# Kernel tuning notes

Hardware: AMD Instinct MI355X
Metric: run time of the kernel (lower is better)

Reference implementation:

```python
import jax, jax.numpy as jnp
import numpy as np

DIM = 2048
K_DIM = 2048
Q_HEADS = 16
KV_HEADS = 4
HEAD_DIM = DIM // Q_HEADS  # 128
KV_DIM = HEAD_DIM * KV_HEADS
ROPE_THETA = 10000.0


def _rope_cos_sin(seq_len, head_dim):
    inv = 1.0 / (ROPE_THETA ** (np.arange(0, head_dim, 2).astype(np.float32) / head_dim))
    t = np.arange(seq_len, dtype=np.float32)
    freqs = np.outer(t, inv)  # (n, head_dim/2)
    return jnp.asarray(np.cos(freqs)), jnp.asarray(np.sin(freqs))


def _apply_rope(x, cos, sin):
    # x: (b, n, h, d); interleaved complex pairs as in torch.view_as_complex
    b, n, h, d = x.shape
    xr, xi = x[..., 0::2], x[..., 1::2]
    c = cos[None, :, None, :]
    s = sin[None, :, None, :]
    yr = xr * c - xi * s
    yi = xr * s + xi * c
    return jnp.stack([yr, yi], axis=-1).reshape(b, n, h, d)


def setup_inputs() -> dict:
    key = jax.random.key(0)
    ks = jax.random.split(key, 11)
    B, N = 2, 2048
    std_q = DIM ** -0.5
    std_k = K_DIM ** -0.5
    return {
        "query": jax.random.normal(ks[0], (B, N, DIM), jnp.float32),
        "key": jax.random.normal(ks[1], (B, N, K_DIM), jnp.float32),
        "value": jax.random.normal(ks[2], (B, N, K_DIM), jnp.float32),
        "Wq": jax.random.normal(ks[3], (DIM, DIM), jnp.float32) * std_q,
        "bq": jnp.zeros((DIM,), jnp.float32),
        "Wk": jax.random.normal(ks[4], (KV_DIM, K_DIM), jnp.float32) * std_k,
        "bk": jnp.zeros((KV_DIM,), jnp.float32),
        "Wv": jax.random.normal(ks[5], (KV_DIM, K_DIM), jnp.float32) * std_k,
        "bv": jnp.zeros((KV_DIM,), jnp.float32),
        "Wo": jax.random.normal(ks[6], (DIM, DIM), jnp.float32) * std_q,
        "bo": jnp.zeros((DIM,), jnp.float32),
    }


def reference(query, key, value, Wq, bq, Wk, bk, Wv, bv, Wo, bo):
    b, nq, _ = query.shape
    nk = key.shape[1]
    q = (query @ Wq.T + bq).reshape(b, nq, Q_HEADS, HEAD_DIM)
    k = (key @ Wk.T + bk).reshape(b, nk, KV_HEADS, HEAD_DIM)
    v = (value @ Wv.T + bv).reshape(b, nk, KV_HEADS, HEAD_DIM)
    cos, sin = _rope_cos_sin(max(nq, nk), HEAD_DIM)
    q = _apply_rope(q, cos[:nq], sin[:nq])
    k = _apply_rope(k, cos[:nk], sin[:nk])
    g = Q_HEADS // KV_HEADS
    # group query heads: head index hh = h*g + gi uses kv head h
    qg = q.reshape(b, nq, KV_HEADS, g, HEAD_DIM)
    scale = HEAD_DIM ** -0.5
    scores = jnp.einsum('bnhgd,bshd->bhgns', qg, k) * scale
    causal = jnp.tril(jnp.ones((nq, nk), dtype=bool))
    scores = jnp.where(causal, scores, jnp.finfo(scores.dtype).min)
    attn = jax.nn.softmax(scores, axis=-1)
    out = jnp.einsum('bhgns,bshd->bnhgd', attn, v).reshape(b, nq, DIM)
    return out @ Wo.T + bo
```

## Files before the change

### kernel.cpp

```cpp
#include <hip/hip_runtime.h>
#include <hip/hip_bf16.h>
#include <stdint.h>

typedef unsigned short u16;
typedef __bf16 v8bf __attribute__((ext_vector_type(8)));
typedef float f32x4 __attribute__((ext_vector_type(4)));

#define BATCH 2
#define NSEQ  2048
#define DIM_  2048
#define QH    16
#define KVH   4
#define HD    128
#define KVDIM 512
#define QKVS  3072
#define MROWS (BATCH*NSEQ)

__device__ __forceinline__ u16 f2bf(float f) {
  uint32_t u = __builtin_bit_cast(uint32_t, f);
  u += 0x7FFFu + ((u >> 16) & 1u);
  return (u16)(u >> 16);
}
__device__ __forceinline__ float bf2f(u16 h) {
  uint32_t u = ((uint32_t)h) << 16;
  return __builtin_bit_cast(float, u);
}
__device__ __forceinline__ uint32_t cvt_pk_bf16(float lo, float hi) {
  uint32_t r;
  asm("v_cvt_pk_bf16_f32 %0, %1, %2" : "=v"(r) : "v"(lo), "v"(hi));
  return r;
}
__device__ __forceinline__ void gload_lds16(const void* g, void* l) {
  __builtin_amdgcn_global_load_lds((const __attribute__((address_space(1))) void*)g,
                                   (__attribute__((address_space(3))) void*)l, 16, 0, 0);
}

__global__ void k_conv_w(const float* __restrict__ wq, const float* __restrict__ wk,
                         const float* __restrict__ wv, const float* __restrict__ wo,
                         u16* __restrict__ oq, u16* __restrict__ ok,
                         u16* __restrict__ ov, u16* __restrict__ oo) {
  int i = (blockIdx.x * 256 + threadIdx.x) * 4;
  const float* in; u16* out; int e;
  if (i < 4194304)      { in = wq; out = oq; e = i; }
  else if (i < 5242880) { in = wk; out = ok; e = i - 4194304; }
  else if (i < 6291456) { in = wv; out = ov; e = i - 5242880; }
  else                  { in = wo; out = oo; e = i - 6291456; }
  float4 v = *(const float4*)(in + e);
  ushort4 o;
  o.x = f2bf(v.x); o.y = f2bf(v.y); o.z = f2bf(v.z); o.w = f2bf(v.w);
  *(ushort4*)(out + e) = o;
}

__global__ void k_conv_x(const float* __restrict__ q, const float* __restrict__ k,
                         const float* __restrict__ v,
                         u16* __restrict__ oq, u16* __restrict__ ok, u16* __restrict__ ov) {
  int i = (blockIdx.x * 256 + threadIdx.x) * 4;
  int r = i >> 23;
  int e = i & ((1 << 23) - 1);
  const float* in = (r == 0) ? q : (r == 1 ? k : v);
  u16* out = (r == 0) ? oq : (r == 1 ? ok : ov);
  float4 vv = *(const float4*)(in + e);
  ushort4 o;
  o.x = f2bf(vv.x); o.y = f2bf(vv.y); o.z = f2bf(vv.z); o.w = f2bf(vv.w);
  *(ushort4*)(out + e) = o;
}

__global__ void k_rope_table2(float2* __restrict__ tab) {
  int idx = blockIdx.x * 256 + threadIdx.x;
  if (idx < NSEQ * 64) {
    int i = idx & 63;
    float inv = powf(10000.0f, -(float)i / 64.0f);
    float ang = (float)(idx >> 6) * inv;
    tab[idx] = make_float2(cosf(ang), sinf(ang));
  }
}

__global__ __launch_bounds__(256) void k_transpose_v(const u16* __restrict__ vp, u16* __restrict__ vt) {
  __shared__ u16 t[64][72];
  int bn = blockIdx.x, bd = blockIdx.y;
  int tid = threadIdx.x;
  int rrow = tid >> 3;
  int rcol = (tid & 7) * 8;
#pragma unroll
  for (int i = 0; i < 2; ++i) {
    int n = rrow + i * 32;
    ushort4 v0 = *(const ushort4*)(vp + (size_t)(bn * 64 + n) * QKVS + bd * 64 + rcol);
    ushort4 v1 = *(const ushort4*)(vp + (size_t)(bn * 64 + n) * QKVS + bd * 64 + rcol + 4);
    *(ushort4*)&t[n][rcol] = v0;
    *(ushort4*)&t[n][rcol + 4] = v1;
  }
  __syncthreads();
  int b = bn >> 5;
  int nbase = (bn & 31) * 64;
#pragma unroll
  for (int i = 0; i < 2; ++i) {
    int dl = rrow + i * 32;
    int dglob = bd * 64 + dl;
    int kvh = dglob >> 7, dd = dglob & 127;
    ushort4 o0, o1;
    o0.x = t[rcol + 0][dl]; o0.y = t[rcol + 1][dl];
    o0.z = t[rcol + 2][dl]; o0.w = t[rcol + 3][dl];
    o1.x = t[rcol + 4][dl]; o1.y = t[rcol + 5][dl];
    o1.z = t[rcol + 6][dl]; o1.w = t[rcol + 7][dl];
    u16* dst = vt + (((size_t)(b * KVH + kvh) * HD + dd) * NSEQ + nbase + rcol);
    *(ushort4*)dst = o0;
    *(ushort4*)(dst + 4) = o1;
  }
}

__global__ __launch_bounds__(256) void k_gemm_qkv(const u16* __restrict__ xq, const u16* __restrict__ xk,
                                                  const u16* __restrict__ xv,
                                                  const u16* __restrict__ wq, const u16* __restrict__ wk,
                                                  const u16* __restrict__ wv,
                                                  const float* __restrict__ bq, const float* __restrict__ bk,
                                                  const float* __restrict__ bv,
                                                  const float2* __restrict__ tab2, u16* __restrict__ C) {
  __shared__ __align__(16) u16 As[2][128 * 32];
  __shared__ __align__(16) u16 Bs[2][128 * 32];
  int tid = threadIdx.x;
  int l = tid & 63, w = tid >> 6;
  int lg = l >> 4, lr = l & 15;
  int wr = w >> 1, wc = w & 1;
  int bm = blockIdx.x, bn = blockIdx.y;

  const u16* A; const u16* B; const float* bias;
  if (bn < 16)      { A = xq; B = wq + (size_t)(bn * 128) * 2048;        bias = bq + bn * 128; }
  else if (bn < 20) { A = xk; B = wk + (size_t)((bn - 16) * 128) * 2048; bias = bk + (bn - 16) * 128; }
  else              { A = xv; B = wv + (size_t)((bn - 20) * 128) * 2048; bias = bv + (bn - 20) * 128; }

  int srow = tid >> 2;
  int scol = (tid & 3) * 16;

  const char* Ab = (const char*)A + ((size_t)(bm * 128 + srow) * 2048) * 2 + scol;
  const char* Bb = (const char*)B + ((size_t)srow * 2048) * 2 + scol;

#define STG(BUF, KT)                                                            \
  {                                                                             \
    size_t koff = (size_t)(KT) * 64;                                            \
    gload_lds16(Ab + koff, (char*)As[BUF] + srow * 64 + scol);                  \
    gload_lds16(Ab + koff + (size_t)64 * 2048 * 2,                              \
                (char*)As[BUF] + (srow + 64) * 64 + scol);                      \
    gload_lds16(Bb + koff, (char*)Bs[BUF] + srow * 64 + scol);                  \
    gload_lds16(Bb + koff + (size_t)64 * 2048 * 2,                              \
                (char*)Bs[BUF] + (srow + 64) * 64 + scol);                      \
  }

  f32x4 acc[4][4] = {};
  STG(0, 0);
  __syncthreads();
  for (int kt = 0; kt < 64; ++kt) {
    int cur = kt & 1;
    if (kt < 63) STG(cur ^ 1, kt + 1);
    const char* AsB = (const char*)As[cur];
    const char* BsB = (const char*)Bs[cur];
    v8bf af[4], bfr[4];
#pragma unroll
    for (int mi = 0; mi < 4; ++mi)
      af[mi] = *(const v8bf*)(AsB + (wr * 64 + mi * 16 + lr) * 64 + lg * 16);
#pragma unroll
    for (int ni = 0; ni < 4; ++ni)
      bfr[ni] = *(const v8bf*)(BsB + (wc * 64 + ni * 16 + lr) * 64 + lg * 16);
#pragma unroll
    for (int mi = 0; mi < 4; ++mi)
#pragma unroll
      for (int ni = 0; ni < 4; ++ni)
        acc[mi][ni] = __builtin_amdgcn_mfma_f32_16x16x32_bf16(af[mi], bfr[ni], acc[mi][ni], 0, 0, 0);
    __syncthreads();
  }
#undef STG

  bool rope = (bn < 20);
#pragma unroll
  for (int mi = 0; mi < 4; ++mi)
#pragma unroll
    for (int ni = 0; ni < 4; ++ni) {
      int grow0 = bm * 128 + wr * 64 + mi * 16 + lg * 4;
      int lcol = wc * 64 + ni * 16 + lr;
      int gcol = bn * 128 + lcol;
      float bsv = bias[lcol];
      if (rope) {
        int i2 = (gcol & 127) >> 1;
#pragma unroll
        for (int r = 0; r < 4; ++r) {
          float v = acc[mi][ni][r] + bsv;
          float pv = __shfl_xor(v, 1);
          int t = (grow0 + r) & (NSEQ - 1);
          float2 cs = tab2[t * 64 + i2];
          float y = (lr & 1) ? (pv * cs.y + v * cs.x) : (v * cs.x - pv * cs.y);
          C[(size_t)(grow0 + r) * QKVS + gcol] = f2bf(y);
        }
      } else {
#pragma unroll
        for (int r = 0; r < 4; ++r)
          C[(size_t)(grow0 + r) * QKVS + gcol] = f2bf(acc[mi][ni][r] + bsv);
      }
    }
}

__global__ __launch_bounds__(256) void k_gemm_bt(const u16* __restrict__ A, const u16* __restrict__ B,
                                                 const float* __restrict__ bias, float* __restrict__ C,
                                                 int M, int N, int K) {
  __shared__ __align__(16) u16 As[2][128 * 32];
  __shared__ __align__(16) u16 Bs[2][128 * 32];
  int tid = threadIdx.x;
  int l = tid & 63, w = tid >> 6;
  int lg = l >> 4, lr = l & 15;
  int wr = w >> 1, wc = w & 1;
  int bm = blockIdx.x, bn = blockIdx.y;

  int srow = tid >> 2;
  int scol = (tid & 3) * 16;

  const char* Ab = (const char*)A + ((size_t)(bm * 128 + srow) * K) * 2 + scol;
  const char* Bb = (const char*)B + ((size_t)(bn * 128 + srow) * K) * 2 + scol;

#define STG(BUF, KT)                                                            \
  {                                                                             \
    size_t koff = (size_t)(KT) * 64;                                            \
    gload_lds16(Ab + koff, (char*)As[BUF] + srow * 64 + scol);                  \
    gload_lds16(Ab + koff + (size_t)64 * K * 2,                                 \
                (char*)As[BUF] + (srow + 64) * 64 + scol);                      \
    gload_lds16(Bb + koff, (char*)Bs[BUF] + srow * 64 + scol);                  \
    gload_lds16(Bb + koff + (size_t)64 * K * 2,                                 \
                (char*)Bs[BUF] + (srow + 64) * 64 + scol);                      \
  }

  f32x4 acc[4][4] = {};
  int ksteps = K >> 5;
  STG(0, 0);
  __syncthreads();
  for (int kt = 0; kt < ksteps; ++kt) {
    int cur = kt & 1;
    if (kt + 1 < ksteps) STG(cur ^ 1, kt + 1);
    const char* AsB = (const char*)As[cur];
    const char* BsB = (const char*)Bs[cur];
    v8bf af[4], bfr[4];
#pragma unroll
    for (int mi = 0; mi < 4; ++mi)
      af[mi] = *(const v8bf*)(AsB + (wr * 64 + mi * 16 + lr) * 64 + lg * 16);
#pragma unroll
    for (int ni = 0; ni < 4; ++ni)
      bfr[ni] = *(const v8bf*)(BsB + (wc * 64 + ni * 16 + lr) * 64 + lg * 16);
#pragma unroll
    for (int mi = 0; mi < 4; ++mi)
#pragma unroll
      for (int ni = 0; ni < 4; ++ni)
        acc[mi][ni] = __builtin_amdgcn_mfma_f32_16x16x32_bf16(af[mi], bfr[ni], acc[mi][ni], 0, 0, 0);
    __syncthreads();
  }
#undef STG

#pragma unroll
  for (int mi = 0; mi < 4; ++mi)
#pragma unroll
    for (int ni = 0; ni < 4; ++ni) {
      int grow0 = bm * 128 + wr * 64 + mi * 16 + lg * 4;
      int gcol = bn * 128 + wc * 64 + ni * 16 + lr;
      float bsv = bias[gcol];
#pragma unroll
      for (int r = 0; r < 4; ++r)
        C[(size_t)(grow0 + r) * N + gcol] = acc[mi][ni][r] + bsv;
    }
}

__global__ __launch_bounds__(256, 2) void k_attn(const u16* __restrict__ q, const u16* __restrict__ k,
                                                 const u16* __restrict__ vt, u16* __restrict__ out) {
  __shared__ __align__(16) u16 Ks[64 * 128];
  __shared__ __align__(16) u16 Vs[128 * 64];

  int tid = threadIdx.x;
  int l = tid & 63, w = tid >> 6;
  int lg = l >> 4, lr = l & 15;
  int h = blockIdx.y, b = blockIdx.z;
  int kvh = h >> 2;
  const float SCL2 = 0.12752551286084109f;
  const float THR2 = 11.541560327111708f;

  const char* kbase = (const char*)k + ((size_t)(b * NSEQ) * QKVS + kvh * HD) * 2;
  const char* vbase = (const char*)vt + ((size_t)(b * KVH + kvh) * HD) * NSEQ * 2;
  char* KsB = (char*)Ks;
  char* VsB = (char*)Vs;

  int krow0 = tid >> 4;
  int kcol = (tid & 15) * 16;
  int vrow0 = tid >> 3;
  int vcol = (tid & 7) * 16;

  v8bf kr[4], vr[4];

#define LOADKV(KT)                                                                          \
  {                                                                                         \
    _Pragma("unroll") for (int i = 0; i < 4; ++i)                                           \
        kr[i] = *(const v8bf*)(kbase + (size_t)((KT) * 64 + krow0 + i * 16) * QKVS * 2 + kcol); \
    _Pragma("unroll") for (int i = 0; i < 4; ++i)                                           \
        vr[i] = *(const v8bf*)(vbase + (size_t)(vrow0 + i * 32) * NSEQ * 2 + (size_t)(KT) * 128 + vcol); \
  }
#define WRITEKV()                                                                           \
  {                                                                                         \
    _Pragma("unroll") for (int i = 0; i < 4; ++i) {                                         \
      int kvl = krow0 + i * 16;                                                             \
      int prow = (kvl & 32) + ((kvl & 4) << 2) + ((kvl & 24) >> 1) + (kvl & 3);             \
      *(v8bf*)(KsB + prow * 256 + (kcol ^ ((prow & 7) << 4))) = kr[i];                      \
    }                                                                                       \
    _Pragma("unroll") for (int i = 0; i < 4; ++i) {                                         \
      int row = vrow0 + i * 32;                                                             \
      *(v8bf*)(VsB + row * 128 + (vcol ^ ((row & 7) << 4))) = vr[i];                        \
    }                                                                                       \
  }

  for (int pass = 0; pass < 2; ++pass) {
    int qt = pass ? (31 - blockIdx.x) : blockIdx.x;
    int q0 = qt * 64 + w * 16;

    const char* qb = (const char*)q + ((size_t)(b * NSEQ + q0 + lr) * QKVS + h * HD) * 2;
    v8bf qf[4];
#pragma unroll
    for (int kk = 0; kk < 4; ++kk) qf[kk] = *(const v8bf*)(qb + kk * 64 + lg * 16);

    f32x4 od[8] = {};
    float m2 = -INFINITY, lsum = 0.f;
    int qrow = q0 + lr;

    int ktmax = qt;
    LOADKV(0);
    WRITEKV();
    __syncthreads();

    for (int kt = 0; kt <= ktmax; ++kt) {
      if (kt < ktmax) LOADKV(kt + 1);

      f32x4 st[4];
      __builtin_amdgcn_s_setprio(1);
#pragma unroll
      for (int nt = 0; nt < 4; ++nt) {
        f32x4 a = {};
#pragma unroll
        for (int kk = 0; kk < 4; ++kk) {
          int krow = nt * 16 + lr;
          v8bf kf = *(const v8bf*)(KsB + krow * 256 + ((kk * 64 + lg * 16) ^ ((krow & 7) << 4)));
          a = __builtin_amdgcn_mfma_f32_16x16x32_bf16(kf, qf[kk], a, 0, 0, 0);
        }
        st[nt] = a;
      }
      __builtin_amdgcn_s_setprio(0);

      if (kt == ktmax) {
#pragma unroll
        for (int nt = 0; nt < 4; ++nt)
#pragma unroll
          for (int r = 0; r < 4; ++r) {
            int kv = kt * 64 + (nt >> 1) * 32 + lg * 8 + ((nt & 1) << 2) + r;
            if (kv > qrow) st[nt][r] = -1e30f;
          }
      }

      float mx = -1e30f;
#pragma unroll
      for (int nt = 0; nt < 4; ++nt)
#pragma unroll
        for (int r = 0; r < 4; ++r) mx = fmaxf(mx, st[nt][r]);
      mx = fmaxf(mx, __shfl_xor(mx, 16));
      mx = fmaxf(mx, __shfl_xor(mx, 32));
      float mx2 = mx * SCL2;

      if (!__all(mx2 - m2 <= THR2)) {
        float nm2 = fmaxf(m2, mx2);
        float corrf = exp2f(m2 - nm2);
        m2 = nm2;
        lsum *= corrf;
#pragma unroll
        for (int r = 0; r < 4; ++r) {
          float cb = __shfl(corrf, lg * 4 + r);
#pragma unroll
          for (int dt = 0; dt < 8; ++dt) od[dt][r] *= cb;
        }
      }

      float rs = 0.f;
#pragma unroll
      for (int nt = 0; nt < 4; ++nt)
#pragma unroll
        for (int r = 0; r < 4; ++r) {
          float pv = exp2f(fmaf(st[nt][r], SCL2, -m2));
          st[nt][r] = pv;
          rs += pv;
        }
      rs += __shfl_xor(rs, 16);
      rs += __shfl_xor(rs, 32);
      lsum += rs;

      uint32_t pk[4][2];
#pragma unroll
      for (int nt = 0; nt < 4; ++nt)
#pragma unroll
        for (int s = 0; s < 2; ++s)
          pk[nt][s] = cvt_pk_bf16(st[nt][2 * s], st[nt][2 * s + 1]);

      __builtin_amdgcn_s_setprio(1);
#pragma unroll
      for (int kc = 0; kc < 2; ++kc) {
        union { uint32_t u[4]; v8bf v; } pfu;
        pfu.u[0] = pk[2 * kc][0];
        pfu.u[1] = pk[2 * kc][1];
        pfu.u[2] = pk[2 * kc + 1][0];
        pfu.u[3] = pk[2 * kc + 1][1];
#pragma unroll
        for (int dt = 0; dt < 8; ++dt) {
          int vrow = dt * 16 + lr;
          v8bf vf = *(const v8bf*)(VsB + vrow * 128 + ((kc * 64 + lg * 16) ^ ((vrow & 7) << 4)));
          od[dt] = __builtin_amdgcn_mfma_f32_16x16x32_bf16(pfu.v, vf, od[dt], 0, 0, 0);
        }
      }
      __builtin_amdgcn_s_setprio(0);

      __syncthreads();
      if (kt < ktmax) WRITEKV();
      __syncthreads();
    }

#pragma unroll
    for (int r = 0; r < 4; ++r) {
      float ls = __shfl(lsum, lg * 4 + r);
      float inv = 1.0f / ls;
      int qr = q0 + lg * 4 + r;
      char* ob = (char*)out + ((size_t)(b * NSEQ + qr) * DIM_ + h * HD) * 2;
#pragma unroll
      for (int dt = 0; dt < 8; ++dt)
        *(u16*)(ob + (dt * 16 + lr) * 2) = f2bf(od[dt][r] * inv);
    }
  }
#undef LOADKV
#undef WRITEKV
}

extern "C" void kernel_launch(void* const* d_in, const int* in_sizes, int n_in,
                              void* d_out, int out_size, void* d_ws, size_t ws_size,
                              hipStream_t stream) {
  const float* query = (const float*)d_in[0];
  const float* key_ = (const float*)d_in[1];
  const float* value = (const float*)d_in[2];
  const float* Wq = (const float*)d_in[3];
  const float* bq = (const float*)d_in[4];
  const float* Wk = (const float*)d_in[5];
  const float* bk = (const float*)d_in[6];
  const float* Wv = (const float*)d_in[7];
  const float* bv = (const float*)d_in[8];
  const float* Wo = (const float*)d_in[9];
  const float* bo = (const float*)d_in[10];

  char* ws = (char*)d_ws;
  u16* wq_bf = (u16*)(ws + 0);
  u16* wk_bf = (u16*)(ws + 8388608);
  u16* wv_bf = (u16*)(ws + 10485760);
  u16* wo_bf = (u16*)(ws + 12582912);
  float2* tab2 = (float2*)(ws + 20971520);
  u16* xq = (u16*)(ws + 22020096);
  u16* xk = (u16*)(ws + 38797312);
  u16* xv = (u16*)(ws + 55574528);
  u16* qkvproj = (u16*)(ws + 72351744);
  u16* vt = xq;
  u16* attno = xk;

  k_conv_w<<<dim3(10240), 256, 0, stream>>>(Wq, Wk, Wv, Wo, wq_bf, wk_bf, wv_bf, wo_bf);
  k_conv_x<<<dim3(24576), 256, 0, stream>>>(query, key_, value, xq, xk, xv);
  k_rope_table2<<<dim3(NSEQ * 64 / 256), 256, 0, stream>>>(tab2);

  k_gemm_qkv<<<dim3(MROWS / 128, QKVS / 128), 256, 0, stream>>>(xq, xk, xv, wq_bf, wk_bf, wv_bf,
                                                                bq, bk, bv, tab2, qkvproj);

  k_transpose_v<<<dim3(MROWS / 64, KVDIM / 64), 256, 0, stream>>>(qkvproj + 2560, vt);

  k_attn<<<dim3(NSEQ / 128, QH, BATCH), 256, 0, stream>>>(qkvproj, qkvproj + 2048, vt, attno);

  k_gemm_bt<<<dim3(MROWS / 128, DIM_ / 128), 256, 0, stream>>>(attno, wo_bf, bo, (float*)d_out, MROWS, DIM_, DIM_);
}
```

Baseline: 232.5 us.

## Double-buffer K/V tiles in attention and merge init kernels into one launch

The attention kernel now keeps two LDS buffers for K and V, so the next tile is written into the alternate buffer and one of the two __syncthreads per iteration goes away. Separately, the weight conversion, input conversion and RoPE table kernels are merged into a single k_init launch to cut launch overhead. The double buffer doubles attention LDS to 64 KB per block, which may limit how many blocks fit per CU under launch_bounds(256,2).

```diff
diff --git a/kernel.cpp b/kernel.cpp
--- a/kernel.cpp
+++ b/kernel.cpp
@@ -21,10 +21,6 @@
   u += 0x7FFFu + ((u >> 16) & 1u);
   return (u16)(u >> 16);
 }
-__device__ __forceinline__ float bf2f(u16 h) {
-  uint32_t u = ((uint32_t)h) << 16;
-  return __builtin_bit_cast(float, u);
-}
 __device__ __forceinline__ uint32_t cvt_pk_bf16(float lo, float hi) {
   uint32_t r;
   asm("v_cvt_pk_bf16_f32 %0, %1, %2" : "=v"(r) : "v"(lo), "v"(hi));
@@ -35,43 +31,44 @@
                                    (__attribute__((address_space(3))) void*)l, 16, 0, 0);
 }
 
-__global__ void k_conv_w(const float* __restrict__ wq, const float* __restrict__ wk,
-                         const float* __restrict__ wv, const float* __restrict__ wo,
-                         u16* __restrict__ oq, u16* __restrict__ ok,
-                         u16* __restrict__ ov, u16* __restrict__ oo) {
-  int i = (blockIdx.x * 256 + threadIdx.x) * 4;
-  const float* in; u16* out; int e;
-  if (i < 4194304)      { in = wq; out = oq; e = i; }
-  else if (i < 5242880) { in = wk; out = ok; e = i - 4194304; }
-  else if (i < 6291456) { in = wv; out = ov; e = i - 5242880; }
-  else                  { in = wo; out = oo; e = i - 6291456; }
-  float4 v = *(const float4*)(in + e);
-  ushort4 o;
-  o.x = f2bf(v.x); o.y = f2bf(v.y); o.z = f2bf(v.z); o.w = f2bf(v.w);
-  *(ushort4*)(out + e) = o;
-}
-
-__global__ void k_conv_x(const float* __restrict__ q, const float* __restrict__ k,
-                         const float* __restrict__ v,
-                         u16* __restrict__ oq, u16* __restrict__ ok, u16* __restrict__ ov) {
-  int i = (blockIdx.x * 256 + threadIdx.x) * 4;
-  int r = i >> 23;
-  int e = i & ((1 << 23) - 1);
-  const float* in = (r == 0) ? q : (r == 1 ? k : v);
-  u16* out = (r == 0) ? oq : (r == 1 ? ok : ov);
-  float4 vv = *(const float4*)(in + e);
-  ushort4 o;
-  o.x = f2bf(vv.x); o.y = f2bf(vv.y); o.z = f2bf(vv.z); o.w = f2bf(vv.w);
-  *(ushort4*)(out + e) = o;
-}
-
-__global__ void k_rope_table2(float2* __restrict__ tab) {
-  int idx = blockIdx.x * 256 + threadIdx.x;
-  if (idx < NSEQ * 64) {
-    int i = idx & 63;
-    float inv = powf(10000.0f, -(float)i / 64.0f);
-    float ang = (float)(idx >> 6) * inv;
-    tab[idx] = make_float2(cosf(ang), sinf(ang));
+__global__ void k_init(const float* __restrict__ q, const float* __restrict__ k,
+                       const float* __restrict__ v,
+                       const float* __restrict__ wq, const float* __restrict__ wk,
+                       const float* __restrict__ wv, const float* __restrict__ wo,
+                       u16* __restrict__ xq, u16* __restrict__ xk, u16* __restrict__ xv,
+                       u16* __restrict__ oq, u16* __restrict__ ok,
+                       u16* __restrict__ ov, u16* __restrict__ oo,
+                       float2* __restrict__ tab) {
+  int bid = blockIdx.x;
+  if (bid < 24576) {
+    int i = (bid * 256 + threadIdx.x) * 4;
+    int r = i >> 23;
+    int e = i & ((1 << 23) - 1);
+    const float* in = (r == 0) ? q : (r == 1 ? k : v);
+    u16* out = (r == 0) ? xq : (r == 1 ? xk : xv);
+    float4 vv = *(const float4*)(in + e);
+    ushort4 o;
+    o.x = f2bf(vv.x); o.y = f2bf(vv.y); o.z = f2bf(vv.z); o.w = f2bf(vv.w);
+    *(ushort4*)(out + e) = o;
+  } else if (bid < 34816) {
+    int i = ((bid - 24576) * 256 + threadIdx.x) * 4;
+    const float* in; u16* out; int e;
+    if (i < 4194304)      { in = wq; out = oq; e = i; }
+    else if (i < 5242880) { in = wk; out = ok; e = i - 4194304; }
+    else if (i < 6291456) { in = wv; out = ov; e = i - 5242880; }
+    else                  { in = wo; out = oo; e = i - 6291456; }
+    float4 vv = *(const float4*)(in + e);
+    ushort4 o;
+    o.x = f2bf(vv.x); o.y = f2bf(vv.y); o.z = f2bf(vv.z); o.w = f2bf(vv.w);
+    *(ushort4*)(out + e) = o;
+  } else {
+    int idx = (bid - 34816) * 256 + threadIdx.x;
+    if (idx < NSEQ * 64) {
+      int i = idx & 63;
+      float inv = powf(10000.0f, -(float)i / 64.0f);
+      float ang = (float)(idx >> 6) * inv;
+      tab[idx] = make_float2(cosf(ang), sinf(ang));
+    }
   }
 }
 
@@ -265,8 +262,8 @@
 
 __global__ __launch_bounds__(256, 2) void k_attn(const u16* __restrict__ q, const u16* __restrict__ k,
                                                  const u16* __restrict__ vt, u16* __restrict__ out) {
-  __shared__ __align__(16) u16 Ks[64 * 128];
-  __shared__ __align__(16) u16 Vs[128 * 64];
+  __shared__ __align__(16) u16 Ks[2][64 * 128];
+  __shared__ __align__(16) u16 Vs[2][128 * 64];
 
   int tid = threadIdx.x;
   int l = tid & 63, w = tid >> 6;
@@ -278,8 +275,6 @@
 
   const char* kbase = (const char*)k + ((size_t)(b * NSEQ) * QKVS + kvh * HD) * 2;
   const char* vbase = (const char*)vt + ((size_t)(b * KVH + kvh) * HD) * NSEQ * 2;
-  char* KsB = (char*)Ks;
-  char* VsB = (char*)Vs;
 
   int krow0 = tid >> 4;
   int kcol = (tid & 15) * 16;
@@ -295,16 +290,18 @@
     _Pragma("unroll") for (int i = 0; i < 4; ++i)                                           \
         vr[i] = *(const v8bf*)(vbase + (size_t)(vrow0 + i * 32) * NSEQ * 2 + (size_t)(KT) * 128 + vcol); \
   }
-#define WRITEKV()                                                                           \
+#define WRITEKV(BUF)                                                                        \
   {                                                                                         \
+    char* KsB_ = (char*)Ks[BUF];                                                            \
+    char* VsB_ = (char*)Vs[BUF];                                                            \
     _Pragma("unroll") for (int i = 0; i < 4; ++i) {                                         \
       int kvl = krow0 + i * 16;                                                             \
       int prow = (kvl & 32) + ((kvl & 4) << 2) + ((kvl & 24) >> 1) + (kvl & 3);             \
-      *(v8bf*)(KsB + prow * 256 + (kcol ^ ((prow & 7) << 4))) = kr[i];                      \
+      *(v8bf*)(KsB_ + prow * 256 + (kcol ^ ((prow & 7) << 4))) = kr[i];                     \
     }                                                                                       \
     _Pragma("unroll") for (int i = 0; i < 4; ++i) {                                         \
       int row = vrow0 + i * 32;                                                             \
-      *(v8bf*)(VsB + row * 128 + (vcol ^ ((row & 7) << 4))) = vr[i];                        \
+      *(v8bf*)(VsB_ + row * 128 + (vcol ^ ((row & 7) << 4))) = vr[i];                       \
     }                                                                                       \
   }
 
@@ -323,11 +320,14 @@
 
     int ktmax = qt;
     LOADKV(0);
-    WRITEKV();
+    WRITEKV(0);
     __syncthreads();
 
     for (int kt = 0; kt <= ktmax; ++kt) {
+      int cur = kt & 1;
       if (kt < ktmax) LOADKV(kt + 1);
+      const char* KsB = (const char*)Ks[cur];
+      const char* VsB = (const char*)Vs[cur];
 
       f32x4 st[4];
       __builtin_amdgcn_s_setprio(1);
@@ -413,8 +413,7 @@
       }
       __builtin_amdgcn_s_setprio(0);
 
-      __syncthreads();
-      if (kt < ktmax) WRITEKV();
+      if (kt < ktmax) WRITEKV(cur ^ 1);
       __syncthreads();
     }
 
@@ -461,9 +460,8 @@
   u16* vt = xq;
   u16* attno = xk;
 
-  k_conv_w<<<dim3(10240), 256, 0, stream>>>(Wq, Wk, Wv, Wo, wq_bf, wk_bf, wv_bf, wo_bf);
-  k_conv_x<<<dim3(24576), 256, 0, stream>>>(query, key_, value, xq, xk, xv);
-  k_rope_table2<<<dim3(NSEQ * 64 / 256), 256, 0, stream>>>(tab2);
+  k_init<<<dim3(35328), 256, 0, stream>>>(query, key_, value, Wq, Wk, Wv, Wo,
+                                          xq, xk, xv, wq_bf, wk_bf, wv_bf, wo_bf, tab2);
 
   k_gemm_qkv<<<dim3(MROWS / 128, QKVS / 128), 256, 0, stream>>>(xq, xk, xv, wq_bf, wk_bf, wv_bf,
                                                                 bq, bk, bv, tab2, qkvproj);
```

After: 229.3 us (median of 2 runs). No clear change (-1.3%).
